# Optimization experiments

Measured on AMD Instinct MI355X. Metric: run time of the kernel, lower is better.

Reference implementation:

```python
import math
import jax, jax.numpy as jnp
import numpy as np

# ---- static config (from init_kwargs) ----
B = 4
FH, FW = 480, 640          # frame size
NSEM = 16
C_OBS = 4 + NSEM           # 20 obs channels (rgb, depth, sem)
C_FEAT = 1 + NSEM          # 17 splatted feature channels
RES = 5.0                  # map resolution cm
VR = 100                   # vision range (cells)
MAXH, MINH = 72, -8        # int(360/5), int(-40/5)
HZ = MAXH - MINH           # 80 height bins
MAP_CELLS = 480            # (4800//2)//5
AGENT_H = 88.0             # camera_height*100
FOV = 79.0
N = FH * FW                # du_scale = 1
MAP_T, EXP_T, CAT_T = 1.0, 1.0, 5.0
DEG = 57.29577951308232
MIN_Z, MAX_Z = 13, 25      # int(25/5 - min_h), int((agent_h+1)/5 - min_h)
X1, X2 = 190, 290          # map crop window
Y1, Y2 = 240, 340


def setup_inputs() -> dict:
    key = jax.random.key(0)
    k1, k2, k3, k4, k5 = jax.random.split(key, 5)
    obs = jax.random.uniform(k1, (B, C_OBS, FH, FW), jnp.float32)
    obs = obs.at[:, 3].multiply(500.0)  # depth channel in cm
    pose_obs = jax.random.normal(k2, (B, 3), jnp.float32) * 0.1
    maps_last = jax.random.uniform(k3, (B, C_OBS, MAP_CELLS, MAP_CELLS), jnp.float32)
    poses_last = jax.random.normal(k4, (B, 3), jnp.float32) * 0.3 \
        + jnp.array([12.0, 12.0, 0.0], jnp.float32)  # near map center (meters, deg)
    sh = jax.random.normal(k5, (B, N, 4), jnp.float32) * 0.1  # SH coeffs per point
    return {"obs": obs, "pose_obs": pose_obs, "maps_last": maps_last,
            "poses_last": poses_last, "sh": sh}


def _affine_grid(theta, H, W):
    # align_corners=True affine grid; theta: (bs, 2, 3) -> (bs, H, W, 2)
    ys = jnp.linspace(-1.0, 1.0, H, dtype=jnp.float32)
    xs = jnp.linspace(-1.0, 1.0, W, dtype=jnp.float32)
    gx, gy = jnp.meshgrid(xs, ys)                       # (H, W)
    base = jnp.stack([gx, gy, jnp.ones_like(gx)], -1)   # (H, W, 3)
    return jnp.einsum('bij,hwj->bhwi', theta, base)


def _grid_sample(img, grid):
    # bilinear, zeros padding, align_corners=True. img: (bs,C,H,W), grid: (bs,H,W,2)
    Bs, C, H, W = img.shape
    x = (grid[..., 0] + 1.0) * (W - 1) / 2.0
    y = (grid[..., 1] + 1.0) * (H - 1) / 2.0
    x0 = jnp.floor(x); y0 = jnp.floor(y)
    x1 = x0 + 1.0; y1 = y0 + 1.0

    def one(img_b, xb, yb, x0b, y0b, x1b, y1b):
        def tap(ix, iy):
            valid = ((ix >= 0) & (ix < W) & (iy >= 0) & (iy < H)).astype(img_b.dtype)
            ic = jnp.clip(ix, 0, W - 1).astype(jnp.int32)
            jc = jnp.clip(iy, 0, H - 1).astype(jnp.int32)
            return img_b[:, jc, ic] * valid[None]        # (C,H,W)
        w00 = (x1b - xb) * (y1b - yb)
        w01 = (xb - x0b) * (y1b - yb)
        w10 = (x1b - xb) * (yb - y0b)
        w11 = (xb - x0b) * (yb - y0b)
        return (tap(x0b, y0b) * w00[None] + tap(x1b, y0b) * w01[None]
                + tap(x0b, y1b) * w10[None] + tap(x1b, y1b) * w11[None])

    return jax.vmap(one)(img, x, y, x0, y0, x1, y1)


def _splat_one(feat_b, coords_b):
    # trilinear scatter-add splat (du.splat_feat_nd). feat_b: (C_FEAT, N), coords_b: (3, N) in [-1,1]
    GD = (VR, VR, HZ)
    grid = jnp.zeros((C_FEAT, VR * VR * HZ), jnp.float32)
    pos = [coords_b[d] * GD[d] / 2.0 + GD[d] / 2.0 for d in range(3)]
    for ix in ((0, 0, 0), (0, 0, 1), (0, 1, 0), (0, 1, 1),
               (1, 0, 0), (1, 0, 1), (1, 1, 0), (1, 1, 1)):
        idx = jnp.zeros((N,), jnp.float32)
        w = jnp.ones((N,), jnp.float32)
        for d in range(3):
            p = jnp.floor(pos[d]) + ix[d]
            safe = ((p > 0) & (p < GD[d])).astype(jnp.float32)
            w = w * (1.0 - jnp.abs(pos[d] - p)) * safe
            idx = idx * GD[d] + p * safe
        grid = grid.at[:, idx.astype(jnp.int32)].add(feat_b * w[None, :])
    return grid


def _forward(obs, pose_obs, maps_last, poses_last, sh):
    bs = obs.shape[0]
    depth = obs[:, 3]                                   # (bs, FH, FW)

    # --- point cloud from depth (du.get_point_cloud_from_z_t) ---
    f = (FW / 2.0) / math.tan(math.radians(FOV / 2.0))
    xc = (FW - 1) / 2.0
    zc = (FH - 1) / 2.0
    gx = jnp.arange(FW, dtype=jnp.float32)
    gz = jnp.arange(FH - 1, -1, -1, dtype=jnp.float32)
    X = (gx[None, None, :] - xc) * depth / f
    Z = (gz[None, :, None] - zc) * depth / f
    # camera view transform (elev=0 -> identity rot, z += agent_h) then
    # shift_loc pose transform (angle pi/2 -> identity rot, x += vr*res//2)
    x_s = X + float(VR * int(RES) // 2)
    y_s = depth
    z_s = Z + AGENT_H

    # --- normalize to [-1,1] voxel coords ---
    xn = (x_s / RES - float(VR // 2)) / VR * 2.0
    yn = (y_s / RES - float(VR // 2)) / VR * 2.0
    zn = (z_s / RES - float((MAXH + MINH) // 2)) / (MAXH - MINH) * 2.0
    coords = jnp.stack([xn, yn, zn], axis=1).reshape(bs, 3, N)
    coords = jnp.clip(coords, -1.0, 1.0)

    # --- features (channel 0 = ones occupancy, rest = semantics; du_scale=1 so avgpool is identity) ---
    feat = jnp.concatenate(
        [jnp.ones((bs, 1, N), jnp.float32), obs[:, 4:].reshape(bs, NSEM, N)], axis=1)
    sh_mean = jnp.mean(sh, axis=2)                      # (bs, N)
    enh = feat * (1.0 + sh_mean[:, None, :])

    # --- voxel splat + round, swap the two xy grid dims (matches .transpose(2,3)) ---
    vox = jax.vmap(_splat_one)(enh, coords)
    vox = jnp.round(vox).reshape(bs, C_FEAT, VR, VR, HZ).transpose(0, 1, 3, 2, 4)

    # --- height projections ---
    agent_proj = vox[..., MIN_Z:MAX_Z].sum(-1)          # (bs, C_FEAT, VR, VR)
    all_proj = vox.sum(-1)
    fp_map_pred = jnp.clip(agent_proj[:, 0:1] / MAP_T, 0.0, 1.0)
    fp_exp_pred = jnp.clip(all_proj[:, 0:1] / EXP_T, 0.0, 1.0)

    # --- write into egocentric map ---
    av = jnp.zeros((bs, C_OBS, MAP_CELLS, MAP_CELLS), jnp.float32)
    av = av.at[:, 0:1, Y1:Y2, X1:X2].set(fp_map_pred)
    av = av.at[:, 1:2, Y1:Y2, X1:X2].set(fp_exp_pred)
    av = av.at[:, 4:, Y1:Y2, X1:X2].set(jnp.clip(agent_proj[:, 1:] / CAT_T, 0.0, 1.0))

    # --- pose integration ---
    t0 = poses_last[:, 2] / DEG
    y_new = poses_last[:, 1] + pose_obs[:, 0] * jnp.sin(t0) + pose_obs[:, 1] * jnp.cos(t0)
    x_new = poses_last[:, 0] + pose_obs[:, 0] * jnp.cos(t0) - pose_obs[:, 1] * jnp.sin(t0)
    t_new = poses_last[:, 2] + pose_obs[:, 2] * DEG
    t_new = jnp.fmod(t_new - 180.0, 360.0) + 180.0
    t_new = jnp.fmod(t_new + 180.0, 360.0) - 180.0
    current_poses = jnp.stack([x_new, y_new, t_new], axis=1)

    # --- spatial transform of egocentric map into allocentric frame ---
    stc = jax.lax.stop_gradient(current_poses)          # matches .clone().detach()
    half = float(MAP_CELLS // 2)                        # 240
    st_xy = -(stc[:, :2] * 100.0 / RES - half) / half
    st_t = (90.0 - stc[:, 2]) * (math.pi / 180.0)
    cos_t, sin_t = jnp.cos(st_t), jnp.sin(st_t)
    zeros = jnp.zeros_like(cos_t); ones = jnp.ones_like(cos_t)
    theta1 = jnp.stack([jnp.stack([cos_t, -sin_t, zeros], 1),
                        jnp.stack([sin_t, cos_t, zeros], 1)], 1)    # (bs,2,3)
    theta2 = jnp.stack([jnp.stack([ones, zeros, st_xy[:, 0]], 1),
                        jnp.stack([zeros, ones, st_xy[:, 1]], 1)], 1)
    rot_grid = _affine_grid(theta1, MAP_CELLS, MAP_CELLS)
    trans_grid = _affine_grid(theta2, MAP_CELLS, MAP_CELLS)
    rotated = _grid_sample(av, rot_grid)
    translated = _grid_sample(rotated, trans_grid)

    map_pred = jnp.maximum(maps_last, translated)
    # pose_pred aliases poses_last which is mutated in-place in torch -> equals current_poses
    return fp_map_pred, map_pred, current_poses, current_poses


def reference(obs, pose_obs, maps_last, poses_last, sh):
    return _forward(obs, pose_obs, maps_last, poses_last, sh)
```

## Files before the change

### kernel.cpp

```cpp
#include <hip/hip_runtime.h>
#include <math.h>

#define FHh 480
#define FWw 640
#define NPIX (FHh*FWw)
#define NSEMC 16
#define COBS 20
#define MAPC 480
#define VRc 100
#define HZc 80
#define MINZc 13
#define MAXZc 25
#define ZW 12
#define NB 4
#define NBINS_DIM 101
#define NBINS_ROW 101
#define COUNTS_PAD 40960
#define BANDMAX 600000
#define NTOT (NB*NPIX)

__global__ void pose_kernel(const float* __restrict__ pose_obs,
                            const float* __restrict__ poses_last,
                            float* __restrict__ out_p1,
                            float* __restrict__ out_p2,
                            float* __restrict__ params)
{
    int b = threadIdx.x;
    if (b >= NB) return;
    float pl0 = poses_last[b*3+0], pl1 = poses_last[b*3+1], pl2 = poses_last[b*3+2];
    float po0 = pose_obs[b*3+0],  po1 = pose_obs[b*3+1],  po2 = pose_obs[b*3+2];
    const float DEGf = 57.29577951308232f;
    float t0 = pl2 / DEGf;
    float s = sinf(t0), c = cosf(t0);
    float y_new = pl1 + po0*s + po1*c;
    float x_new = pl0 + po0*c - po1*s;
    float t_new = pl2 + po2*DEGf;
    t_new = fmodf(t_new - 180.0f, 360.0f) + 180.0f;
    t_new = fmodf(t_new + 180.0f, 360.0f) - 180.0f;
    out_p1[b*3+0]=x_new; out_p1[b*3+1]=y_new; out_p1[b*3+2]=t_new;
    out_p2[b*3+0]=x_new; out_p2[b*3+1]=y_new; out_p2[b*3+2]=t_new;
    float sx = -(((x_new*100.0f)/5.0f - 240.0f)/240.0f);
    float sy = -(((y_new*100.0f)/5.0f - 240.0f)/240.0f);
    float st_t = (90.0f - t_new) * 0.017453292519943295f;
    params[b*4+0] = cosf(st_t);
    params[b*4+1] = sinf(st_t);
    params[b*4+2] = sx;
    params[b*4+3] = sy;
}

__device__ __forceinline__ float4 pixel_pos(const float* __restrict__ obsb,
                                            const float* __restrict__ sh,
                                            int b, int n, float fconst)
{
    int col = n % FWw, row = n / FWw;
    float depth = obsb[3*NPIX + n];
    const float4 s4 = ((const float4*)sh)[(size_t)b*NPIX + n];
    float sm = (((s4.x + s4.y) + s4.z) + s4.w) / 4.0f;
    float factor = 1.0f + sm;

    float X = ((float)col - 319.5f) * depth / fconst;
    float Z = ((float)(FHh-1-row) - 239.5f) * depth / fconst;
    float x_s = X + 250.0f;
    float z_s = Z + 88.0f;
    float xn = (x_s/5.0f - 50.0f)/100.0f*2.0f;
    float yn = (depth/5.0f - 50.0f)/100.0f*2.0f;
    float zn = (z_s/5.0f - 32.0f)/80.0f*2.0f;
    xn = fminf(fmaxf(xn,-1.0f),1.0f);
    yn = fminf(fmaxf(yn,-1.0f),1.0f);
    zn = fminf(fmaxf(zn,-1.0f),1.0f);
    float pos0 = (xn*100.0f)/2.0f + 50.0f;
    float pos1 = (yn*100.0f)/2.0f + 50.0f;
    float pos2 = (zn*80.0f)/2.0f + 40.0f;
    return make_float4(pos0, pos1, pos2, factor);
}

__device__ __forceinline__ bool dim_ok(float p, int GD)
{
    int f = (int)floorf(p);
    float fr = p - (float)f;
    bool t0 = (f > 0) && (f < GD);
    bool t1 = (f + 1 < GD) && (fr > 0.0f);
    return t0 || t1;
}

__global__ void bin_count_kernel(const float* __restrict__ obs,
                                 const float* __restrict__ sh,
                                 int* __restrict__ auxBid,
                                 int* __restrict__ counts,
                                 int* __restrict__ countsB,
                                 float fconst)
{
    int g = blockIdx.x*blockDim.x + threadIdx.x;
    if (g >= NTOT) return;
    int b = g / NPIX, n = g % NPIX;
    const float* obsb = obs + (size_t)b*COBS*NPIX;
    float4 P = pixel_pos(obsb, sh, b, n, fconst);

    bool ok = dim_ok(P.x, VRc) && dim_ok(P.y, VRc) && dim_ok(P.z, HZc);
    if (!ok) { auxBid[g] = -1; return; }

    int f0 = (int)floorf(P.x);
    int f1 = (int)floorf(P.y);
    int bid = (b*NBINS_DIM + f0)*NBINS_ROW + f1;
    atomicAdd(&counts[bid], 1);
    bool band = (P.z > 12.0f) && (P.z < 25.0f);
    if (band) atomicAdd(&countsB[bid], 1);
    auxBid[g] = band ? (bid | (1<<30)) : bid;
}

__global__ void scan_kernel(int* __restrict__ base)
{
    int* cnt = base + (size_t)blockIdx.x * 2 * COUNTS_PAD;
    int* wrk = cnt + COUNTS_PAD;
    __shared__ int part[1024];
    int t = threadIdx.x;
    const int CHUNK = COUNTS_PAD / 1024;
    int bo = t*CHUNK;
    int s = 0;
    for (int k = 0; k < CHUNK; ++k) s += cnt[bo+k];
    part[t] = s;
    __syncthreads();
    for (int off = 1; off < 1024; off <<= 1) {
        int v = (t >= off) ? part[t-off] : 0;
        __syncthreads();
        part[t] += v;
        __syncthreads();
    }
    int run = part[t] - s;
    for (int k = 0; k < CHUNK; ++k) {
        int c = cnt[bo+k];
        cnt[bo+k] = run;
        wrk[bo+k] = run;
        run += c;
    }
}

__global__ void scatter_kernel(const float* __restrict__ obs,
                               const float* __restrict__ sh,
                               const int* __restrict__ auxBid,
                               int* __restrict__ offsetsWork,
                               int* __restrict__ offsetsWorkB,
                               float4* __restrict__ payloadPos,
                               float4* __restrict__ bandPos,
                               float4* __restrict__ bandSem,
                               float fconst)
{
    int g = blockIdx.x*blockDim.x + threadIdx.x;
    if (g >= NTOT) return;
    int v = auxBid[g];
    if (v < 0) return;
    int bid  = v & 0x3FFFFFFF;
    bool band = (v >> 30) & 1;

    int b = g / NPIX, n = g % NPIX;
    const float* obsb = obs + (size_t)b*COBS*NPIX;
    float4 P = pixel_pos(obsb, sh, b, n, fconst);

    int dst = atomicAdd(&offsetsWork[bid], 1);
    payloadPos[dst] = P;

    if (band) {
        int dstB = atomicAdd(&offsetsWorkB[bid], 1);
        if (dstB < BANDMAX) {
            bandPos[dstB] = P;
            float4* bs = bandSem + (size_t)dstB*4;
            #pragma unroll
            for (int q = 0; q < 4; ++q) {
                float4 e;
                e.x = obsb[(4 + 4*q + 0)*NPIX + n] * P.w;
                e.y = obsb[(4 + 4*q + 1)*NPIX + n] * P.w;
                e.z = obsb[(4 + 4*q + 2)*NPIX + n] * P.w;
                e.w = obsb[(4 + 4*q + 3)*NPIX + n] * P.w;
                bs[q] = e;
            }
        }
    }
}

__global__ __launch_bounds__(64)
void gather_kernel(const float4* __restrict__ payloadPos,
                   const int* __restrict__ offsets,
                   const float4* __restrict__ bandPos,
                   const float* __restrict__ bandSemF,
                   const int* __restrict__ offsetsB,
                   float* __restrict__ avwin,
                   float* __restrict__ fp_out)
{
    int cell = blockIdx.x;
    int b = blockIdx.y;
    int tid = threadIdx.x;
    int i = cell % VRc, j = cell / VRc;

    __shared__ float acc[HZc + NSEMC*ZW];
    for (int k = tid; k < HZc + NSEMC*ZW; k += 64) acc[k] = 0.0f;
    __syncthreads();

    if (i > 0 && j > 0) {
        #pragma unroll
        for (int fi = 0; fi < 2; ++fi) {
            int f0r = i - 1 + fi;
            int rb = (b*NBINS_DIM + f0r)*NBINS_ROW;
            int s = offsets[rb + j - 1];
            int e = offsets[rb + j + 1];
            for (int idx = s + tid; idx < e; idx += 64) {
                float4 P = payloadPos[idx];
                float wx = 1.0f - fabsf(P.x - (float)i);
                float wy = 1.0f - fabsf(P.y - (float)j);
                float wxy = wx * wy;
                if (wxy <= 0.0f) continue;
                int qA = (int)floorf(P.z), qB = qA + 1;
                float fz = P.z - (float)qA;
                if (qA > 0 && qA < HZc) {
                    float w = wxy * (1.0f - fz);
                    if (w > 0.0f) atomicAdd(&acc[qA], P.w * w);
                }
                if (qB > 0 && qB < HZc) {
                    float w = wxy * fz;
                    if (w > 0.0f) atomicAdd(&acc[qB], P.w * w);
                }
            }
            int sB = offsetsB[rb + j - 1];
            int eB = offsetsB[rb + j + 1];
            int c = tid & 15;
            for (int idx = sB + (tid >> 4); idx < eB; idx += 4) {
                float4 P = bandPos[idx];
                float wx = 1.0f - fabsf(P.x - (float)i);
                float wy = 1.0f - fabsf(P.y - (float)j);
                float wxy = wx * wy;
                if (wxy <= 0.0f) continue;
                int qA = (int)floorf(P.z), qB = qA + 1;
                float fz = P.z - (float)qA;
                float w0 = (qA >= MINZc && qA < MAXZc) ? wxy * (1.0f - fz) : 0.0f;
                float w1 = (qB >= MINZc && qB < MAXZc) ? wxy * fz          : 0.0f;
                if (w0 <= 0.0f && w1 <= 0.0f) continue;
                float ev = bandSemF[(size_t)idx*16 + c];
                if (w0 > 0.0f) atomicAdd(&acc[HZc + c*ZW + (qA - MINZc)], ev * w0);
                if (w1 > 0.0f) atomicAdd(&acc[HZc + c*ZW + (qB - MINZc)], ev * w1);
            }
        }
    }
    __syncthreads();

    float* avb = avwin + (size_t)b*18*10000;
    if (tid < NSEMC) {
        float sum = 0.0f;
        #pragma unroll
        for (int z = 0; z < ZW; ++z) sum += rintf(acc[HZc + tid*ZW + z]);
        avb[(2+tid)*10000 + cell] = fminf(fmaxf(sum/5.0f, 0.0f), 1.0f);
    } else if (tid == 16) {
        float agent = 0.0f;
        #pragma unroll
        for (int z = MINZc; z < MAXZc; ++z) agent += rintf(acc[z]);
        float v = fminf(fmaxf(agent, 0.0f), 1.0f);
        avb[0*10000 + cell] = v;
        fp_out[(size_t)b*10000 + cell] = v;
    } else if (tid == 17) {
        float all = 0.0f;
        for (int z = 0; z < HZc; ++z) all += rintf(acc[z]);
        avb[1*10000 + cell] = fminf(fmaxf(all, 0.0f), 1.0f);
    }
}

__device__ __forceinline__ float grid1d(int i) {
    return (float)(-1.0 + (double)i * (2.0/479.0));
}

__global__ void map_kernel(const float* __restrict__ maps_last,
                           const float* __restrict__ avwin,
                           const float* __restrict__ params,
                           float* __restrict__ map_out)
{
    int t = blockIdx.x*blockDim.x + threadIdx.x;
    if (t >= NB*MAPC*MAPC) return;
    int w = t % MAPC;
    int h = (t / MAPC) % MAPC;
    int b = t / (MAPC*MAPC);
    float ct = params[b*4+0], st = params[b*4+1];
    float sx = params[b*4+2], sy = params[b*4+3];

    float xg = grid1d(w) + sx;
    float yg = grid1d(h) + sy;
    float xt = ((xg + 1.0f)*479.0f)/2.0f;
    float yt = ((yg + 1.0f)*479.0f)/2.0f;
    float xf = floorf(xt), yf = floorf(yt);

    float acc[18];
    #pragma unroll
    for (int k=0;k<18;k++) acc[k]=0.0f;
    const float* avb = avwin + (size_t)b*18*10000;

    #pragma unroll
    for (int oy=0; oy<2; ++oy) {
        #pragma unroll
        for (int ox=0; ox<2; ++ox) {
            float qx = xf + (float)ox, qy = yf + (float)oy;
            if (!(qx >= 0.0f && qx < 480.0f && qy >= 0.0f && qy < 480.0f)) continue;
            float wo = (ox ? (xt - xf) : (xf + 1.0f - xt))
                     * (oy ? (yt - yf) : (yf + 1.0f - yt));
            int oxi = (int)qx, oyi = (int)qy;
            float gxr = grid1d(oxi), gyr = grid1d(oyi);
            float xr = ct*gxr - st*gyr;
            float yr = st*gxr + ct*gyr;
            float xp = ((xr + 1.0f)*479.0f)/2.0f;
            float yp = ((yr + 1.0f)*479.0f)/2.0f;
            float xpf = floorf(xp), ypf = floorf(yp);
            float R[18];
            #pragma unroll
            for (int k=0;k<18;k++) R[k]=0.0f;
            #pragma unroll
            for (int iy=0; iy<2; ++iy) {
                #pragma unroll
                for (int ix=0; ix<2; ++ix) {
                    float rx = xpf + (float)ix, ry = ypf + (float)iy;
                    if (!(rx >= 0.0f && rx < 480.0f && ry >= 0.0f && ry < 480.0f)) continue;
                    int rxi = (int)rx, ryi = (int)ry;
                    if (ryi < 240 || ryi >= 340 || rxi < 190 || rxi >= 290) continue;
                    float wi = (ix ? (xp - xpf) : (xpf + 1.0f - xp))
                             * (iy ? (yp - ypf) : (ypf + 1.0f - yp));
                    const float* p = avb + (ryi-240)*VRc + (rxi-190);
                    #pragma unroll
                    for (int k=0;k<18;k++) R[k] += wi * p[k*10000];
                }
            }
            #pragma unroll
            for (int k=0;k<18;k++) acc[k] += wo * R[k];
        }
    }

    #pragma unroll
    for (int c=0;c<COBS;c++) {
        size_t o = (((size_t)b*COBS + c)*MAPC + h)*MAPC + w;
        float tv = (c==0) ? acc[0] : (c==1) ? acc[1] : (c>=4) ? acc[c-2] : 0.0f;
        map_out[o] = fmaxf(maps_last[o], tv);
    }
}

extern "C" void kernel_launch(void* const* d_in, const int* in_sizes, int n_in,
                              void* d_out, int out_size, void* d_ws, size_t ws_size,
                              hipStream_t stream)
{
    const float* obs        = (const float*)d_in[0];
    const float* pose_obs   = (const float*)d_in[1];
    const float* maps_last  = (const float*)d_in[2];
    const float* poses_last = (const float*)d_in[3];
    const float* sh         = (const float*)d_in[4];
    float* out = (float*)d_out;

    float* fp_out  = out;
    float* map_out = out + 40000;
    float* poses1  = out + 40000 + 18432000;
    float* poses2  = poses1 + 12;

    float* params = (float*)d_ws;
    float* avwin  = params + 16;

    float4* payloadPos  = (float4*)map_out;
    int*    auxBid      = (int*)(map_out + 4915200);
    int*    counts      = (int*)(map_out + 6144000);
    int*    offsetsWork = counts + COUNTS_PAD;
    int*    countsB     = counts + 2*COUNTS_PAD;
    int*    offsetsWorkB= counts + 3*COUNTS_PAD;
    float4* bandPos     = (float4*)(map_out + 6144000 + 4*COUNTS_PAD);
    float4* bandSem     = (float4*)(map_out + 6144000 + 4*COUNTS_PAD + (size_t)BANDMAX*4);

    double rad = 39.5 * 0.017453292519943295;
    float fconst = (float)(320.0 / tan(rad));

    hipLaunchKernelGGL(pose_kernel, dim3(1), dim3(64), 0, stream,
                       pose_obs, poses_last, poses1, poses2, params);

    hipMemsetAsync(counts, 0, (size_t)4*COUNTS_PAD*sizeof(int), stream);

    hipLaunchKernelGGL(bin_count_kernel, dim3((NTOT+255)/256), dim3(256), 0, stream,
                       obs, sh, auxBid, counts, countsB, fconst);

    hipLaunchKernelGGL(scan_kernel, dim3(2), dim3(1024), 0, stream, counts);

    hipLaunchKernelGGL(scatter_kernel, dim3((NTOT+255)/256), dim3(256), 0, stream,
                       obs, sh, auxBid, offsetsWork, offsetsWorkB,
                       payloadPos, bandPos, bandSem, fconst);

    hipLaunchKernelGGL(gather_kernel, dim3(10000, NB), dim3(64), 0, stream,
                       payloadPos, counts, bandPos, (const float*)bandSem, countsB,
                       avwin, fp_out);

    hipLaunchKernelGGL(map_kernel, dim3((NB*MAPC*MAPC+255)/256), dim3(256), 0, stream,
                       maps_last, avwin, params, map_out);
}
```

Baseline: 904.2 us.

## Splat occupancy directly with global atomics and gather band semantics per row

The all-height occupancy channels are now accumulated by scattering each point's trilinear weights straight into a dense global voxel grid with atomics. This removes the full counting-sort pass for every point (counts, payload scatter and per-cell gather). Only band points are still sorted, and they are gathered by blocks that each cover half a row of 50 cells, with shared-memory accumulators. In exchange the change adds heavy global atomic contention on the occupancy grid and a larger memset.

```diff
diff --git a/kernel.cpp b/kernel.cpp
--- a/kernel.cpp
+++ b/kernel.cpp
@@ -12,6 +12,7 @@
 #define MINZc 13
 #define MAXZc 25
 #define ZW 12
+#define ZWP 13
 #define NB 4
 #define NBINS_DIM 101
 #define NBINS_ROW 101
@@ -83,12 +84,12 @@
     return t0 || t1;
 }
 
-__global__ void bin_count_kernel(const float* __restrict__ obs,
-                                 const float* __restrict__ sh,
-                                 int* __restrict__ auxBid,
-                                 int* __restrict__ counts,
-                                 int* __restrict__ countsB,
-                                 float fconst)
+__global__ __launch_bounds__(256)
+void project_kernel(const float* __restrict__ obs,
+                    const float* __restrict__ sh,
+                    float* __restrict__ occ,
+                    int* __restrict__ countsB,
+                    float fconst)
 {
     int g = blockIdx.x*blockDim.x + threadIdx.x;
     if (g >= NTOT) return;
@@ -96,21 +97,44 @@
     const float* obsb = obs + (size_t)b*COBS*NPIX;
     float4 P = pixel_pos(obsb, sh, b, n, fconst);
 
-    bool ok = dim_ok(P.x, VRc) && dim_ok(P.y, VRc) && dim_ok(P.z, HZc);
-    if (!ok) { auxBid[g] = -1; return; }
-
     int f0 = (int)floorf(P.x);
     int f1 = (int)floorf(P.y);
-    int bid = (b*NBINS_DIM + f0)*NBINS_ROW + f1;
-    atomicAdd(&counts[bid], 1);
-    bool band = (P.z > 12.0f) && (P.z < 25.0f);
-    if (band) atomicAdd(&countsB[bid], 1);
-    auxBid[g] = band ? (bid | (1<<30)) : bid;
+    int f2 = (int)floorf(P.z);
+    float* occb = occ + (size_t)b*VRc*VRc*HZc;
+
+    #pragma unroll
+    for (int dj = 0; dj < 2; ++dj) {
+        int tj = f1 + dj;
+        if (tj < 1 || tj > 99) continue;
+        float wy = 1.0f - fabsf(P.y - (float)tj);
+        if (wy <= 0.0f) continue;
+        #pragma unroll
+        for (int di = 0; di < 2; ++di) {
+            int ti = f0 + di;
+            if (ti < 1 || ti > 99) continue;
+            float wx = 1.0f - fabsf(P.x - (float)ti);
+            if (wx <= 0.0f) continue;
+            float wxy = wx * wy;
+            #pragma unroll
+            for (int dz = 0; dz < 2; ++dz) {
+                int q = f2 + dz;
+                if (q < 1 || q > 79) continue;
+                float w = wxy * (1.0f - fabsf(P.z - (float)q));
+                if (w > 0.0f)
+                    atomicAdd(&occb[((size_t)tj*VRc + ti)*HZc + q], P.w * w);
+            }
+        }
+    }
+
+    if (dim_ok(P.x, VRc) && dim_ok(P.y, VRc) && P.z > 12.0f && P.z < 25.0f) {
+        int bid = (b*NBINS_DIM + f1)*NBINS_ROW + f0;
+        atomicAdd(&countsB[bid], 1);
+    }
 }
 
 __global__ void scan_kernel(int* __restrict__ base)
 {
-    int* cnt = base + (size_t)blockIdx.x * 2 * COUNTS_PAD;
+    int* cnt = base;
     int* wrk = cnt + COUNTS_PAD;
     __shared__ int part[1024];
     int t = threadIdx.x;
@@ -135,129 +159,125 @@
     }
 }
 
-__global__ void scatter_kernel(const float* __restrict__ obs,
-                               const float* __restrict__ sh,
-                               const int* __restrict__ auxBid,
-                               int* __restrict__ offsetsWork,
-                               int* __restrict__ offsetsWorkB,
-                               float4* __restrict__ payloadPos,
-                               float4* __restrict__ bandPos,
-                               float4* __restrict__ bandSem,
-                               float fconst)
+__global__ __launch_bounds__(256)
+void band_scatter_kernel(const float* __restrict__ obs,
+                         const float* __restrict__ sh,
+                         int* __restrict__ offsetsWork,
+                         float4* __restrict__ bandPos,
+                         float4* __restrict__ bandSem,
+                         float fconst)
 {
     int g = blockIdx.x*blockDim.x + threadIdx.x;
     if (g >= NTOT) return;
-    int v = auxBid[g];
-    if (v < 0) return;
-    int bid  = v & 0x3FFFFFFF;
-    bool band = (v >> 30) & 1;
-
     int b = g / NPIX, n = g % NPIX;
     const float* obsb = obs + (size_t)b*COBS*NPIX;
     float4 P = pixel_pos(obsb, sh, b, n, fconst);
 
+    if (!(dim_ok(P.x, VRc) && dim_ok(P.y, VRc) && P.z > 12.0f && P.z < 25.0f))
+        return;
+    int f0 = (int)floorf(P.x);
+    int f1 = (int)floorf(P.y);
+    int bid = (b*NBINS_DIM + f1)*NBINS_ROW + f0;
     int dst = atomicAdd(&offsetsWork[bid], 1);
-    payloadPos[dst] = P;
-
-    if (band) {
-        int dstB = atomicAdd(&offsetsWorkB[bid], 1);
-        if (dstB < BANDMAX) {
-            bandPos[dstB] = P;
-            float4* bs = bandSem + (size_t)dstB*4;
-            #pragma unroll
-            for (int q = 0; q < 4; ++q) {
-                float4 e;
-                e.x = obsb[(4 + 4*q + 0)*NPIX + n] * P.w;
-                e.y = obsb[(4 + 4*q + 1)*NPIX + n] * P.w;
-                e.z = obsb[(4 + 4*q + 2)*NPIX + n] * P.w;
-                e.w = obsb[(4 + 4*q + 3)*NPIX + n] * P.w;
-                bs[q] = e;
+    if (dst >= BANDMAX) return;
+    bandPos[dst] = P;
+    float4* bs = bandSem + (size_t)dst*4;
+    #pragma unroll
+    for (int q = 0; q < 4; ++q) {
+        float4 e;
+        e.x = obsb[(4 + 4*q + 0)*NPIX + n] * P.w;
+        e.y = obsb[(4 + 4*q + 1)*NPIX + n] * P.w;
+        e.z = obsb[(4 + 4*q + 2)*NPIX + n] * P.w;
+        e.w = obsb[(4 + 4*q + 3)*NPIX + n] * P.w;
+        bs[q] = e;
+    }
+}
+
+__global__ __launch_bounds__(256)
+void gather_rows_kernel(const float* __restrict__ occ,
+                        const float4* __restrict__ bandPos,
+                        const float* __restrict__ bandSemF,
+                        const int* __restrict__ offsetsB,
+                        float* __restrict__ avwin,
+                        float* __restrict__ fp_out)
+{
+    int j  = blockIdx.x >> 1;
+    int i0 = (blockIdx.x & 1) * 50;
+    int b  = blockIdx.y;
+    int tid = threadIdx.x;
+
+    __shared__ float accSem[50*NSEMC*ZWP];
+    __shared__ float occL[50*81];
+
+    for (int k = tid; k < 50*NSEMC*ZWP; k += 256) accSem[k] = 0.0f;
+    __syncthreads();
+
+    if (j >= 1) {
+        int f0lo = (i0 == 0) ? 0 : (i0 - 1);
+        int f0hi = i0 + 49;
+        int tmin = (i0 == 0) ? 1 : i0;
+        int cgrp = tid & 15;
+        #pragma unroll
+        for (int seg = 0; seg < 2; ++seg) {
+            int f1r = j - 1 + seg;
+            int rbB = (b*NBINS_DIM + f1r)*NBINS_ROW;
+            int s = offsetsB[rbB + f0lo];
+            int e = offsetsB[rbB + f0hi + 1];
+            if (s < 0) s = 0;
+            if (e > BANDMAX) e = BANDMAX;
+            for (int idx = s + (tid >> 4); idx < e; idx += 16) {
+                float4 P = bandPos[idx];
+                float wy = 1.0f - fabsf(P.y - (float)j);
+                if (wy <= 0.0f) continue;
+                float ev = bandSemF[(size_t)idx*16 + cgrp];
+                int f0c = (int)floorf(P.x);
+                int qA  = (int)floorf(P.z);
+                #pragma unroll
+                for (int di = 0; di < 2; ++di) {
+                    int ti = f0c + di;
+                    if (ti < tmin || ti > i0 + 49) continue;
+                    float wx = 1.0f - fabsf(P.x - (float)ti);
+                    if (wx <= 0.0f) continue;
+                    float wxy = wx * wy;
+                    int base = ((ti - i0)*NSEMC + cgrp)*ZWP - MINZc;
+                    #pragma unroll
+                    for (int dz = 0; dz < 2; ++dz) {
+                        int q = qA + dz;
+                        if (q < MINZc || q >= MAXZc) continue;
+                        float w = wxy * (1.0f - fabsf(P.z - (float)q));
+                        if (w > 0.0f) atomicAdd(&accSem[base + q], ev * w);
+                    }
+                }
             }
         }
     }
-}
-
-__global__ __launch_bounds__(64)
-void gather_kernel(const float4* __restrict__ payloadPos,
-                   const int* __restrict__ offsets,
-                   const float4* __restrict__ bandPos,
-                   const float* __restrict__ bandSemF,
-                   const int* __restrict__ offsetsB,
-                   float* __restrict__ avwin,
-                   float* __restrict__ fp_out)
-{
-    int cell = blockIdx.x;
-    int b = blockIdx.y;
-    int tid = threadIdx.x;
-    int i = cell % VRc, j = cell / VRc;
-
-    __shared__ float acc[HZc + NSEMC*ZW];
-    for (int k = tid; k < HZc + NSEMC*ZW; k += 64) acc[k] = 0.0f;
+
+    const float* orow = occ + (((size_t)b*VRc + j)*VRc + i0)*HZc;
+    for (int k = tid; k < 50*HZc; k += 256)
+        occL[(k/HZc)*81 + (k%HZc)] = orow[k];
     __syncthreads();
 
-    if (i > 0 && j > 0) {
+    float* avb = avwin + (size_t)b*18*10000;
+    int cell0 = j*100 + i0;
+
+    for (int c = tid; c < 50; c += 256) {
+        float agent = 0.0f, all = 0.0f;
+        for (int z = 0; z < HZc; ++z) {
+            float r = rintf(occL[c*81 + z]);
+            all += r;
+            if (z >= MINZc && z < MAXZc) agent += r;
+        }
+        float va = fminf(fmaxf(agent, 0.0f), 1.0f);
+        avb[cell0 + c] = va;
+        fp_out[(size_t)b*10000 + cell0 + c] = va;
+        avb[10000 + cell0 + c] = fminf(fmaxf(all, 0.0f), 1.0f);
+    }
+    for (int t = tid; t < 50*NSEMC; t += 256) {
+        int c = t >> 4, ch = t & 15;
+        float s = 0.0f;
         #pragma unroll
-        for (int fi = 0; fi < 2; ++fi) {
-            int f0r = i - 1 + fi;
-            int rb = (b*NBINS_DIM + f0r)*NBINS_ROW;
-            int s = offsets[rb + j - 1];
-            int e = offsets[rb + j + 1];
-            for (int idx = s + tid; idx < e; idx += 64) {
-                float4 P = payloadPos[idx];
-                float wx = 1.0f - fabsf(P.x - (float)i);
-                float wy = 1.0f - fabsf(P.y - (float)j);
-                float wxy = wx * wy;
-                if (wxy <= 0.0f) continue;
-                int qA = (int)floorf(P.z), qB = qA + 1;
-                float fz = P.z - (float)qA;
-                if (qA > 0 && qA < HZc) {
-                    float w = wxy * (1.0f - fz);
-                    if (w > 0.0f) atomicAdd(&acc[qA], P.w * w);
-                }
-                if (qB > 0 && qB < HZc) {
-                    float w = wxy * fz;
-                    if (w > 0.0f) atomicAdd(&acc[qB], P.w * w);
-                }
-            }
-            int sB = offsetsB[rb + j - 1];
-            int eB = offsetsB[rb + j + 1];
-            int c = tid & 15;
-            for (int idx = sB + (tid >> 4); idx < eB; idx += 4) {
-                float4 P = bandPos[idx];
-                float wx = 1.0f - fabsf(P.x - (float)i);
-                float wy = 1.0f - fabsf(P.y - (float)j);
-                float wxy = wx * wy;
-                if (wxy <= 0.0f) continue;
-                int qA = (int)floorf(P.z), qB = qA + 1;
-                float fz = P.z - (float)qA;
-                float w0 = (qA >= MINZc && qA < MAXZc) ? wxy * (1.0f - fz) : 0.0f;
-                float w1 = (qB >= MINZc && qB < MAXZc) ? wxy * fz          : 0.0f;
-                if (w0 <= 0.0f && w1 <= 0.0f) continue;
-                float ev = bandSemF[(size_t)idx*16 + c];
-                if (w0 > 0.0f) atomicAdd(&acc[HZc + c*ZW + (qA - MINZc)], ev * w0);
-                if (w1 > 0.0f) atomicAdd(&acc[HZc + c*ZW + (qB - MINZc)], ev * w1);
-            }
-        }
-    }
-    __syncthreads();
-
-    float* avb = avwin + (size_t)b*18*10000;
-    if (tid < NSEMC) {
-        float sum = 0.0f;
-        #pragma unroll
-        for (int z = 0; z < ZW; ++z) sum += rintf(acc[HZc + tid*ZW + z]);
-        avb[(2+tid)*10000 + cell] = fminf(fmaxf(sum/5.0f, 0.0f), 1.0f);
-    } else if (tid == 16) {
-        float agent = 0.0f;
-        #pragma unroll
-        for (int z = MINZc; z < MAXZc; ++z) agent += rintf(acc[z]);
-        float v = fminf(fmaxf(agent, 0.0f), 1.0f);
-        avb[0*10000 + cell] = v;
-        fp_out[(size_t)b*10000 + cell] = v;
-    } else if (tid == 17) {
-        float all = 0.0f;
-        for (int z = 0; z < HZc; ++z) all += rintf(acc[z]);
-        avb[1*10000 + cell] = fminf(fmaxf(all, 0.0f), 1.0f);
+        for (int z = 0; z < ZW; ++z) s += rintf(accSem[(c*NSEMC + ch)*ZWP + z]);
+        avb[(2+ch)*10000 + cell0 + c] = fminf(fmaxf(s*0.2f, 0.0f), 1.0f);
     }
 }
 
@@ -354,14 +374,11 @@
     float* params = (float*)d_ws;
     float* avwin  = params + 16;
 
-    float4* payloadPos  = (float4*)map_out;
-    int*    auxBid      = (int*)(map_out + 4915200);
-    int*    counts      = (int*)(map_out + 6144000);
-    int*    offsetsWork = counts + COUNTS_PAD;
-    int*    countsB     = counts + 2*COUNTS_PAD;
-    int*    offsetsWorkB= counts + 3*COUNTS_PAD;
-    float4* bandPos     = (float4*)(map_out + 6144000 + 4*COUNTS_PAD);
-    float4* bandSem     = (float4*)(map_out + 6144000 + 4*COUNTS_PAD + (size_t)BANDMAX*4);
+    float* occ          = map_out;
+    int*   countsB      = (int*)(map_out + 3200000);
+    int*   offsetsWork  = countsB + COUNTS_PAD;
+    float4* bandPos     = (float4*)(map_out + 3200000 + 2*COUNTS_PAD);
+    float4* bandSem     = (float4*)(map_out + 3200000 + 2*COUNTS_PAD + (size_t)BANDMAX*4);
 
     double rad = 39.5 * 0.017453292519943295;
     float fconst = (float)(320.0 / tan(rad));
@@ -369,20 +386,18 @@
     hipLaunchKernelGGL(pose_kernel, dim3(1), dim3(64), 0, stream,
                        pose_obs, poses_last, poses1, poses2, params);
 
-    hipMemsetAsync(counts, 0, (size_t)4*COUNTS_PAD*sizeof(int), stream);
-
-    hipLaunchKernelGGL(bin_count_kernel, dim3((NTOT+255)/256), dim3(256), 0, stream,
-                       obs, sh, auxBid, counts, countsB, fconst);
-
-    hipLaunchKernelGGL(scan_kernel, dim3(2), dim3(1024), 0, stream, counts);
-
-    hipLaunchKernelGGL(scatter_kernel, dim3((NTOT+255)/256), dim3(256), 0, stream,
-                       obs, sh, auxBid, offsetsWork, offsetsWorkB,
-                       payloadPos, bandPos, bandSem, fconst);
-
-    hipLaunchKernelGGL(gather_kernel, dim3(10000, NB), dim3(64), 0, stream,
-                       payloadPos, counts, bandPos, (const float*)bandSem, countsB,
-                       avwin, fp_out);
+    hipMemsetAsync(occ, 0, (size_t)(3200000 + 2*COUNTS_PAD)*sizeof(float), stream);
+
+    hipLaunchKernelGGL(project_kernel, dim3((NTOT+255)/256), dim3(256), 0, stream,
+                       obs, sh, occ, countsB, fconst);
+
+    hipLaunchKernelGGL(scan_kernel, dim3(1), dim3(1024), 0, stream, countsB);
+
+    hipLaunchKernelGGL(band_scatter_kernel, dim3((NTOT+255)/256), dim3(256), 0, stream,
+                       obs, sh, offsetsWork, bandPos, bandSem, fconst);
+
+    hipLaunchKernelGGL(gather_rows_kernel, dim3(200, NB), dim3(256), 0, stream,
+                       occ, bandPos, (const float*)bandSem, countsB, avwin, fp_out);
 
     hipLaunchKernelGGL(map_kernel, dim3((NB*MAPC*MAPC+255)/256), dim3(256), 0, stream,
                        maps_last, avwin, params, map_out);
```

Measured after the change: 1.366 ms. 51.0% more time.
